# Performance work log

Measured on AMD Instinct MI355X. Metric: run time of the kernel, lower is better.

Reference implementation:

```python
import jax, jax.numpy as jnp
import numpy as np
from jax import lax

D_TEMPORAL, D_INNER, D_STATE, D_CONV, DT_RANK = 2, 4, 16, 4, 1
EPS = 1e-5


def setup_inputs() -> dict:
    key = jax.random.key(0)
    ks = jax.random.split(key, 14)
    B, L = 16, 32768
    f = lambda k, s, scale=1.0: jax.random.normal(k, s, jnp.float32) * scale
    dt_b = float(np.log(np.expm1(0.01)))  # softplus^-1(0.01), typical dt init
    A_log = jnp.log(jnp.tile(jnp.arange(1, D_STATE + 1, dtype=jnp.float32), (D_INNER, 1)))
    return {
        "hidden_states": f(ks[0], (B, D_TEMPORAL, L)),
        "norm_w": jnp.ones((D_TEMPORAL,), jnp.float32),
        "in_proj_w": f(ks[1], (2 * D_INNER, D_TEMPORAL), 0.5),
        "conv_w": f(ks[2], (D_INNER, D_CONV), 0.3),
        "conv_b": f(ks[3], (D_INNER,), 0.1),
        "x_proj_w": f(ks[4], (DT_RANK + 2 * D_STATE, D_INNER), 0.3),
        "dt_proj_w": f(ks[5], (D_INNER, DT_RANK), 1.0),
        "dt_proj_b": jnp.full((D_INNER,), dt_b, jnp.float32),
        "A_log": A_log,
        "D": jnp.ones((D_INNER,), jnp.float32),
        "conv_w_b": f(ks[6], (D_INNER, D_CONV), 0.3),
        "conv_b_b": f(ks[7], (D_INNER,), 0.1),
        "x_proj_w_b": f(ks[8], (DT_RANK + 2 * D_STATE, D_INNER), 0.3),
        "dt_proj_w_b": f(ks[9], (D_INNER, DT_RANK), 1.0),
        "dt_proj_b_b": jnp.full((D_INNER,), dt_b, jnp.float32),
        "A_b_log": A_log,
        "D_b": jnp.ones((D_INNER,), jnp.float32),
        "out_proj_w": f(ks[10], (D_TEMPORAL, D_INNER), 0.3),
        "norm_f_w": jnp.ones((D_TEMPORAL,), jnp.float32),
    }


def _silu(x):
    return x * jax.nn.sigmoid(x)


def _rmsnorm(x, w):
    return x * lax.rsqrt(jnp.mean(x * x, axis=-1, keepdims=True) + EPS) * w


def _branch(x, z, conv_w, conv_b, x_proj_w, dt_proj_w, dt_proj_b, A_log, D):
    # x, z: (B, d_inner, L). Causal depthwise conv + silu.
    Bb, d, L = x.shape
    xc = lax.conv_general_dilated(
        x, conv_w[:, None, :], (1,), [(D_CONV - 1, 0)],
        feature_group_count=d, dimension_numbers=("NCH", "OIH", "NCH"))
    u = _silu(xc + conv_b[None, :, None]).transpose(0, 2, 1)      # (B, L, d)
    x_dbl = u @ x_proj_w.T                                        # (B, L, rank+2n)
    dt, Bm, Cm = jnp.split(x_dbl, [DT_RANK, DT_RANK + D_STATE], axis=-1)
    dt = jax.nn.softplus(dt @ dt_proj_w.T + dt_proj_b)            # (B, L, d)
    A = -jnp.exp(A_log)                                           # (d, n)
    dA = jnp.exp(dt[..., None] * A)                               # (B, L, d, n)
    dBu = (dt * u)[..., None] * Bm[:, :, None, :]                 # (B, L, d, n)

    def step(h, inp):
        dA_t, dBu_t, C_t = inp
        h = dA_t * h + dBu_t                                      # (B, d, n)
        return h, jnp.einsum("bdn,bn->bd", h, C_t)

    h0 = jnp.zeros((Bb, d, D_STATE), dtype=u.dtype)
    _, ys = lax.scan(step, h0, (jnp.swapaxes(dA, 0, 1), jnp.swapaxes(dBu, 0, 1), jnp.swapaxes(Cm, 0, 1)))
    y = jnp.swapaxes(ys, 0, 1) + u * D                            # (B, L, d)
    return y * _silu(z.transpose(0, 2, 1))


def _forward(hidden_states, norm_w, in_proj_w, conv_w, conv_b, x_proj_w, dt_proj_w,
             dt_proj_b, A_log, D, conv_w_b, conv_b_b, x_proj_w_b, dt_proj_w_b,
             dt_proj_b_b, A_b_log, D_b, out_proj_w, norm_f_w):
    # hidden_states: (B, T=d_temporal, L); scan runs over L.
    hs = jnp.swapaxes(hidden_states, 1, 2)                        # (B, L, T)
    residual = hs.astype(jnp.float32)
    hs = _rmsnorm(residual, norm_w)
    xz = jnp.swapaxes(hs @ in_proj_w.T, 1, 2)                     # (B, 2*d_inner, L)
    x, z = jnp.split(xz, 2, axis=1)
    y_f = _branch(x, z, conv_w, conv_b, x_proj_w, dt_proj_w, dt_proj_b, A_log, D)
    y_b = _branch(x[..., ::-1], z[..., ::-1], conv_w_b, conv_b_b, x_proj_w_b,
                  dt_proj_w_b, dt_proj_b_b, A_b_log, D_b)
    y = y_f + y_b[:, ::-1, :]                                     # (B, L, d_inner)
    out = y @ out_proj_w.T                                        # (B, L, T)
    out = _rmsnorm(out + residual, norm_f_w)
    return jnp.swapaxes(out, 1, 2)                                # (B, T, L)


def reference(hidden_states, norm_w, in_proj_w, conv_w, conv_b, x_proj_w, dt_proj_w,
              dt_proj_b, A_log, D, conv_w_b, conv_b_b, x_proj_w_b, dt_proj_w_b,
              dt_proj_b_b, A_b_log, D_b, out_proj_w, norm_f_w):
    return _forward(hidden_states, norm_w, in_proj_w, conv_w, conv_b, x_proj_w,
                    dt_proj_w, dt_proj_b, A_log, D, conv_w_b, conv_b_b, x_proj_w_b,
                    dt_proj_w_b, dt_proj_b_b, A_b_log, D_b, out_proj_w, norm_f_w)
```

## Files before the change

kernel.cpp:

```cpp
#include <hip/hip_runtime.h>
#include <hip/hip_bf16.h>
#include <cstdint>

#define BB 16
#define LL 32768
#define NC 512

#define WD_SZ 256
#define XPW 0
#define CVW 132
#define CVB 148
#define DTW 152
#define DTB 156
#define AW  160
#define DW  224
#define G_INPROJ 512
#define G_NORMW 528
#define G_OUTP 530
#define G_NORMF 538
#define FLG 1000

#define PQ_OFF 4096
#define PQ_BYTES ((size_t)BB*2*NC*64*8)
#define HIN_OFF (PQ_OFF + PQ_BYTES)
#define HIN_BYTES ((size_t)BB*2*NC*64*4)
#define PLN_OFF (HIN_OFF + HIN_BYTES)
#define PLN_STRIDE 14336
#define PLN_BYTES ((size_t)BB*NC*PLN_STRIDE)

#define O_DTF 0
#define O_DTB 1088
#define O_DUF 2176
#define O_DUB 2752
#define O_BCF 3328
#define O_BCB 7680
#define O_ZS  12032
#define O_UD  13056

__device__ __forceinline__ float bf2f(unsigned short u){ return __uint_as_float(((unsigned int)u)<<16); }
__device__ __forceinline__ float blo(unsigned int u){ return __uint_as_float(u<<16); }
__device__ __forceinline__ float bhi(unsigned int u){ return __uint_as_float(u & 0xffff0000u); }
__device__ __forceinline__ unsigned short f2bf(float f){
  unsigned int x = __float_as_uint(f);
  x += 0x7fffu + ((x>>16)&1u);
  return (unsigned short)(x>>16);
}
__device__ __forceinline__ unsigned int pack2(float a, float b){
  __hip_bfloat162 h = __float22bfloat162_rn(make_float2(a,b));
  union { __hip_bfloat162 h2; unsigned int u; } cv; cv.h2 = h;
  return cv.u;
}
__device__ __forceinline__ float siluf(float x){
  return x * __builtin_amdgcn_rcpf(1.f + __expf(-x));
}
__device__ __forceinline__ float softplusf_(float x){
  return fmaxf(x,0.f) + 0.69314718056f*__log2f(1.f + __expf(-fabsf(x)));
}

__device__ __forceinline__ float rowsum16(float x){
  union { float f; int i; } a, t;
  a.f = x;
  t.i = __builtin_amdgcn_update_dpp(0, a.i, 0x121, 0xf, 0xf, true); a.f += t.f;
  t.i = __builtin_amdgcn_update_dpp(0, a.i, 0x122, 0xf, 0xf, true); a.f += t.f;
  t.i = __builtin_amdgcn_update_dpp(0, a.i, 0x124, 0xf, 0xf, true); a.f += t.f;
  t.i = __builtin_amdgcn_update_dpp(0, a.i, 0x128, 0xf, 0xf, true); a.f += t.f;
  return a.f;
}

__device__ __forceinline__ float ldw(const void* p, int i, int isf){
  return isf ? ((const float*)p)[i] : bf2f(((const unsigned short*)p)[i]);
}
__device__ __forceinline__ float2 hid2(const void* hid, int isf, int b, int t){
  if (isf){
    const float* p = (const float*)hid;
    return make_float2(p[(size_t)b*2*LL + t], p[(size_t)b*2*LL + LL + t]);
  }
  const unsigned short* p = (const unsigned short*)hid;
  return make_float2(bf2f(p[(size_t)b*2*LL + t]), bf2f(p[(size_t)b*2*LL + LL + t]));
}
__device__ __forceinline__ float4 xrow(const void* __restrict__ hid, int isf,
                                       const float* __restrict__ W, int b, int t){
  float2 h = hid2(hid, isf, b, t);
  float ms = rsqrtf(0.5f*(h.x*h.x + h.y*h.y) + 1e-5f);
  float v0 = h.x*ms*W[G_NORMW], v1 = h.y*ms*W[G_NORMW+1];
  float4 x;
  x.x = W[G_INPROJ+0]*v0 + W[G_INPROJ+1]*v1;
  x.y = W[G_INPROJ+2]*v0 + W[G_INPROJ+3]*v1;
  x.z = W[G_INPROJ+4]*v0 + W[G_INPROJ+5]*v1;
  x.w = W[G_INPROJ+6]*v0 + W[G_INPROJ+7]*v1;
  return x;
}

__device__ __forceinline__ void phaseA(const void* __restrict__ hid, int isf,
    const float* __restrict__ W, int b, int c, int lane,
    unsigned char* smem, float4* xb)
{
  float* dtF = (float*)(smem+O_DTF);
  float* dtB = (float*)(smem+O_DTB);
  unsigned short* duF = (unsigned short*)(smem+O_DUF);
  unsigned short* duB = (unsigned short*)(smem+O_DUB);
  unsigned int* BCF = (unsigned int*)(smem+O_BCF);
  unsigned int* BCB = (unsigned int*)(smem+O_BCB);
  float* zsP = (float*)(smem+O_ZS);
  float* uDP = (float*)(smem+O_UD);
  {
    int t = c*64 + lane;
    float2 h = hid2(hid, isf, b, t);
    float ms = rsqrtf(0.5f*(h.x*h.x + h.y*h.y) + 1e-5f);
    float v0 = h.x*ms*W[G_NORMW], v1 = h.y*ms*W[G_NORMW+1];
    float4 x;
    x.x = W[G_INPROJ+0]*v0 + W[G_INPROJ+1]*v1;
    x.y = W[G_INPROJ+2]*v0 + W[G_INPROJ+3]*v1;
    x.z = W[G_INPROJ+4]*v0 + W[G_INPROJ+5]*v1;
    x.w = W[G_INPROJ+6]*v0 + W[G_INPROJ+7]*v1;
    xb[lane+3] = x;
    float4 z4;
    z4.x = siluf(W[G_INPROJ+ 8]*v0 + W[G_INPROJ+ 9]*v1);
    z4.y = siluf(W[G_INPROJ+10]*v0 + W[G_INPROJ+11]*v1);
    z4.z = siluf(W[G_INPROJ+12]*v0 + W[G_INPROJ+13]*v1);
    z4.w = siluf(W[G_INPROJ+14]*v0 + W[G_INPROJ+15]*v1);
    *(float4*)&zsP[lane*4] = z4;
    if (lane < 3){
      int t2 = c*64 - 3 + lane;
      float4 v = make_float4(0.f,0.f,0.f,0.f);
      if (t2 >= 0) v = xrow(hid, isf, W, b, t2);
      xb[lane] = v;
    }
    if (lane >= 61){
      int t3 = c*64 + lane + 3;
      float4 v = make_float4(0.f,0.f,0.f,0.f);
      if (t3 < LL) v = xrow(hid, isf, W, b, t3);
      xb[lane+6] = v;
    }
  }
  __syncthreads();
  float4 xk0=xb[lane],xk1=xb[lane+1],xk2=xb[lane+2],xk3=xb[lane+3];
  float4 xk4=xb[lane+4],xk5=xb[lane+5],xk6=xb[lane+6];
  float uf[4], ub[4];
  uf[0] = siluf(W[CVB+0] + W[CVW+ 0]*xk0.x + W[CVW+ 1]*xk1.x + W[CVW+ 2]*xk2.x + W[CVW+ 3]*xk3.x);
  uf[1] = siluf(W[CVB+1] + W[CVW+ 4]*xk0.y + W[CVW+ 5]*xk1.y + W[CVW+ 6]*xk2.y + W[CVW+ 7]*xk3.y);
  uf[2] = siluf(W[CVB+2] + W[CVW+ 8]*xk0.z + W[CVW+ 9]*xk1.z + W[CVW+10]*xk2.z + W[CVW+11]*xk3.z);
  uf[3] = siluf(W[CVB+3] + W[CVW+12]*xk0.w + W[CVW+13]*xk1.w + W[CVW+14]*xk2.w + W[CVW+15]*xk3.w);
  const float* Wb = W + WD_SZ;
  ub[0] = siluf(Wb[CVB+0] + Wb[CVW+ 0]*xk6.x + Wb[CVW+ 1]*xk5.x + Wb[CVW+ 2]*xk4.x + Wb[CVW+ 3]*xk3.x);
  ub[1] = siluf(Wb[CVB+1] + Wb[CVW+ 4]*xk6.y + Wb[CVW+ 5]*xk5.y + Wb[CVW+ 6]*xk4.y + Wb[CVW+ 7]*xk3.y);
  ub[2] = siluf(Wb[CVB+2] + Wb[CVW+ 8]*xk6.z + Wb[CVW+ 9]*xk5.z + Wb[CVW+10]*xk4.z + Wb[CVW+11]*xk3.z);
  ub[3] = siluf(Wb[CVB+3] + Wb[CVW+12]*xk6.w + Wb[CVW+13]*xk5.w + Wb[CVW+14]*xk4.w + Wb[CVW+15]*xk3.w);
  *(float4*)&uDP[lane*4] = make_float4(
      uf[0]*W[DW+0]+ub[0]*Wb[DW+0], uf[1]*W[DW+1]+ub[1]*Wb[DW+1],
      uf[2]*W[DW+2]+ub[2]*Wb[DW+2], uf[3]*W[DW+3]+ub[3]*Wb[DW+3]);
  #pragma unroll
  for (int dr=0; dr<2; dr++){
    const float* Wd = W + dr*WD_SZ;
    const float* uu = dr ? ub : uf;
    float* dtp = dr ? dtB : dtF;
    unsigned short* dup = dr ? duB : duF;
    unsigned int* bcp = dr ? BCB : BCF;
    float dtr = Wd[XPW+0]*uu[0]+Wd[XPW+1]*uu[1]+Wd[XPW+2]*uu[2]+Wd[XPW+3]*uu[3];
    #pragma unroll
    for (int d2=0; d2<4; d2++){
      float dt = softplusf_(fmaf(Wd[DTW+d2], dtr, Wd[DTB+d2]));
      dtp[d2*68+lane] = dt;
      dup[d2*72+lane] = f2bf(dt*uu[d2]);
    }
    #pragma unroll
    for (int n=0;n<16;n++){
      float Bn = Wd[XPW+(1+n)*4+0]*uu[0]+Wd[XPW+(1+n)*4+1]*uu[1]
               + Wd[XPW+(1+n)*4+2]*uu[2]+Wd[XPW+(1+n)*4+3]*uu[3];
      float Cn = Wd[XPW+(17+n)*4+0]*uu[0]+Wd[XPW+(17+n)*4+1]*uu[1]
               + Wd[XPW+(17+n)*4+2]*uu[2]+Wd[XPW+(17+n)*4+3]*uu[3];
      bcp[n*68+lane] = pack2(Bn,Cn);
    }
  }
}

__global__ void k_prep(const void* __restrict__ normw, const void* __restrict__ inpj,
    const void* __restrict__ cwf, const void* __restrict__ cbf,
    const void* __restrict__ xpf, const void* __restrict__ dwf,
    const void* __restrict__ dbf, const void* __restrict__ alf,
    const void* __restrict__ ddf,
    const void* __restrict__ cwb, const void* __restrict__ cbb,
    const void* __restrict__ xpb, const void* __restrict__ dwb,
    const void* __restrict__ dbb, const void* __restrict__ alb,
    const void* __restrict__ ddb,
    const void* __restrict__ outp, const void* __restrict__ nfw,
    float* __restrict__ W)
{
  const int isf = (((const unsigned int*)ddf)[0] == 0x3F800000u) ? 1 : 0;
  int t = threadIdx.x;
  for (int i=t;i<132;i+=256){ W[XPW+i]=ldw(xpf,i,isf); W[WD_SZ+XPW+i]=ldw(xpb,i,isf); }
  for (int i=t;i<16;i+=256){ W[CVW+i]=ldw(cwf,i,isf); W[WD_SZ+CVW+i]=ldw(cwb,i,isf); W[G_INPROJ+i]=ldw(inpj,i,isf); }
  for (int i=t;i<4;i+=256){
    W[CVB+i]=ldw(cbf,i,isf); W[WD_SZ+CVB+i]=ldw(cbb,i,isf);
    W[DTW+i]=ldw(dwf,i,isf); W[WD_SZ+DTW+i]=ldw(dwb,i,isf);
    W[DTB+i]=ldw(dbf,i,isf); W[WD_SZ+DTB+i]=ldw(dbb,i,isf);
    W[DW+i] =ldw(ddf,i,isf); W[WD_SZ+DW+i] =ldw(ddb,i,isf);
  }
  for (int i=t;i<64;i+=256){
    W[AW+i]       = -__expf(ldw(alf,i,isf)) * 1.44269504089f;
    W[WD_SZ+AW+i] = -__expf(ldw(alb,i,isf)) * 1.44269504089f;
  }
  for (int i=t;i<8;i+=256) W[G_OUTP+i]=ldw(outp,i,isf);
  for (int i=t;i<2;i+=256){ W[G_NORMW+i]=ldw(normw,i,isf); W[G_NORMF+i]=ldw(nfw,i,isf); }
  if (t==0) W[FLG] = (float)isf;
}

template<bool SPL>
__global__ __launch_bounds__(64) void k_chunk(const void* __restrict__ hid,
    const float* __restrict__ W, float2* __restrict__ PQ,
    unsigned char* __restrict__ planes)
{
  __shared__ __align__(16) unsigned char smem[PLN_STRIDE];
  __shared__ __align__(16) float4 xb[70];
  const int lane = threadIdx.x;
  const int gid  = blockIdx.x;
  const int c    = gid & (NC-1);
  const int b    = gid >> 9;
  const int isf  = (int)W[FLG];

  phaseA(hid, isf, W, b, c, lane, smem, xb);
  __syncthreads();
  if (SPL){
    uint4* gp = (uint4*)(planes + (size_t)gid*PLN_STRIDE);
    const uint4* sp = (const uint4*)smem;
    #pragma unroll
    for (int i=0;i<14;i++) gp[i*64+lane] = sp[i*64+lane];
  }
  const float* dtF = (const float*)(smem+O_DTF);
  const float* dtB = (const float*)(smem+O_DTB);
  const unsigned short* duF = (const unsigned short*)(smem+O_DUF);
  const unsigned short* duB = (const unsigned short*)(smem+O_DUB);
  const unsigned int* BCF = (const unsigned int*)(smem+O_BCF);
  const unsigned int* BCB = (const unsigned int*)(smem+O_BCB);
  const int d = lane>>4, n = lane&15;
  const float Af = W[AW + d*16 + n];
  const float Ab = W[WD_SZ + AW + d*16 + n];
  float Pf=1.f, Qf=0.f, Pb=1.f, Qb=0.f;
  for (int j4=0; j4<16; j4++){
    const int t0f = j4*4, t0b = 60 - j4*4;
    float4 df4 = *(const float4*)&dtF[d*68+t0f];
    float4 db4 = *(const float4*)&dtB[d*68+t0b];
    uint2 uf2 = *(const uint2*)&duF[d*72+t0f];
    uint2 ub2 = *(const uint2*)&duB[d*72+t0b];
    uint4 cf4 = *(const uint4*)&BCF[n*68+t0f];
    uint4 cb4 = *(const uint4*)&BCB[n*68+t0b];
    float dfa[4]={df4.x,df4.y,df4.z,df4.w}, dba[4]={db4.x,db4.y,db4.z,db4.w};
    float duf[4]={blo(uf2.x),bhi(uf2.x),blo(uf2.y),bhi(uf2.y)};
    float dub[4]={blo(ub2.x),bhi(ub2.x),blo(ub2.y),bhi(ub2.y)};
    unsigned int cfa[4]={cf4.x,cf4.y,cf4.z,cf4.w}, cba[4]={cb4.x,cb4.y,cb4.z,cb4.w};
    #pragma unroll
    for (int jr=0; jr<4; jr++){
      float e = exp2f(Af*dfa[jr]);
      Pf *= e;
      Qf = fmaf(Qf, e, duf[jr]*blo(cfa[jr]));
      const int k = 3-jr;
      float eb = exp2f(Ab*dba[k]);
      Pb *= eb;
      Qb = fmaf(Qb, eb, dub[k]*blo(cba[k]));
    }
  }
  PQ[((size_t)(b*2+0)*NC + c)*64 + lane]        = make_float2(Pf,Qf);
  PQ[((size_t)(b*2+1)*NC + (NC-1-c))*64 + lane] = make_float2(Pb,Qb);
}

__global__ __launch_bounds__(256) void k_scan(const float2* __restrict__ PQ, float* __restrict__ hin)
{
  __shared__ float2 seg[4][64];
  const int bd = blockIdx.x;
  const int lane = threadIdx.x & 63;
  const int w = threadIdx.x >> 6;
  const size_t base = (size_t)bd*NC;
  const int c0 = w*128;
  float h = 0.f, R = 1.f;
  for (int cc=0; cc<128; cc+=16){
    float2 v[16];
    #pragma unroll
    for (int k=0;k<16;k++) v[k] = PQ[(base+c0+cc+k)*64+lane];
    #pragma unroll
    for (int k=0;k<16;k++){
      hin[(base+c0+cc+k)*64+lane] = h;
      h = fmaf(v[k].x, h, v[k].y);
      R *= v[k].x;
    }
  }
  seg[w][lane] = make_float2(R, h);
  __syncthreads();
  if (w > 0){
    float init = 0.f;
    #pragma unroll
    for (int s=0; s<3; s++){
      if (s < w){ float2 pq = seg[s][lane]; init = fmaf(pq.x, init, pq.y); }
    }
    float Rr = 1.f;
    for (int cc=0; cc<128; cc+=16){
      float pv[16], hv[16];
      #pragma unroll
      for (int k=0;k<16;k++) pv[k] = PQ[(base+c0+cc+k)*64+lane].x;
      #pragma unroll
      for (int k=0;k<16;k++) hv[k] = hin[(base+c0+cc+k)*64+lane];
      #pragma unroll
      for (int k=0;k<16;k++){
        hin[(base+c0+cc+k)*64+lane] = hv[k] + init*Rr;
        Rr *= pv[k];
      }
    }
  }
}

template<bool LPL>
__global__ __launch_bounds__(64) void k_fused(const void* __restrict__ hid,
    const float* __restrict__ W, const float* __restrict__ hin,
    const unsigned char* __restrict__ planes, void* __restrict__ out)
{
  __shared__ __align__(16) unsigned char smem[PLN_STRIDE];
  __shared__ __align__(16) float ySf[4][68];
  __shared__ __align__(16) float ySb[4][68];
  const int lane = threadIdx.x;
  const int gid  = blockIdx.x;
  const int c    = gid & (NC-1);
  const int b    = gid >> 9;
  const int isf  = (int)W[FLG];

  float hF = hin[((size_t)(b*2+0)*NC + c)*64 + lane];
  float hB = hin[((size_t)(b*2+1)*NC + (NC-1-c))*64 + lane];

  if constexpr (LPL){
    const uint4* gp = (const uint4*)(planes + (size_t)gid*PLN_STRIDE);
    uint4* sp = (uint4*)smem;
    #pragma unroll
    for (int i=0;i<14;i++) sp[i*64+lane] = gp[i*64+lane];
  } else {
    __shared__ __align__(16) float4 xb[70];
    phaseA(hid, isf, W, b, c, lane, smem, xb);
  }
  __syncthreads();

  const float* dtF = (const float*)(smem+O_DTF);
  const float* dtB = (const float*)(smem+O_DTB);
  const unsigned short* duF = (const unsigned short*)(smem+O_DUF);
  const unsigned short* duB = (const unsigned short*)(smem+O_DUB);
  const unsigned int* BCF = (const unsigned int*)(smem+O_BCF);
  const unsigned int* BCB = (const unsigned int*)(smem+O_BCB);
  const float* zsP = (const float*)(smem+O_ZS);
  const float* uDP = (const float*)(smem+O_UD);

  const int d = lane>>4, n = lane&15;
  const float Af = W[AW + d*16 + n];
  const float Ab = W[WD_SZ + AW + d*16 + n];
  for (int j4=0; j4<16; j4++){
    const int t0f = j4*4, t0b = 60 - j4*4;
    float4 df4 = *(const float4*)&dtF[d*68+t0f];
    float4 db4 = *(const float4*)&dtB[d*68+t0b];
    uint2 uf2 = *(const uint2*)&duF[d*72+t0f];
    uint2 ub2 = *(const uint2*)&duB[d*72+t0b];
    uint4 cf4 = *(const uint4*)&BCF[n*68+t0f];
    uint4 cb4 = *(const uint4*)&BCB[n*68+t0b];
    float dfa[4]={df4.x,df4.y,df4.z,df4.w}, dba[4]={db4.x,db4.y,db4.z,db4.w};
    float duf[4]={blo(uf2.x),bhi(uf2.x),blo(uf2.y),bhi(uf2.y)};
    float dub[4]={blo(ub2.x),bhi(ub2.x),blo(ub2.y),bhi(ub2.y)};
    unsigned int cfa[4]={cf4.x,cf4.y,cf4.z,cf4.w}, cba[4]={cb4.x,cb4.y,cb4.z,cb4.w};
    float sF[4], sB[4];
    #pragma unroll
    for (int jr=0; jr<4; jr++){
      float e = exp2f(Af*dfa[jr]);
      hF = fmaf(e, hF, duf[jr]*blo(cfa[jr]));
      sF[jr] = rowsum16(hF*bhi(cfa[jr]));
      const int k = 3-jr;
      float eb = exp2f(Ab*dba[k]);
      hB = fmaf(eb, hB, dub[k]*blo(cba[k]));
      sB[k] = rowsum16(hB*bhi(cba[k]));
    }
    if (n == 0){
      *(float4*)&ySf[d][t0f] = make_float4(sF[0],sF[1],sF[2],sF[3]);
      *(float4*)&ySb[d][t0b] = make_float4(sB[0],sB[1],sB[2],sB[3]);
    }
  }
  __syncthreads();
  {
    int t = c*64 + lane;
    float4 zz = *(const float4*)&zsP[lane*4];
    float4 ud = *(const float4*)&uDP[lane*4];
    float y0 = (ySf[0][lane] + ySb[0][lane] + ud.x) * zz.x;
    float y1 = (ySf[1][lane] + ySb[1][lane] + ud.y) * zz.y;
    float y2 = (ySf[2][lane] + ySb[2][lane] + ud.z) * zz.z;
    float y3 = (ySf[3][lane] + ySb[3][lane] + ud.w) * zz.w;
    float o0 = W[G_OUTP+0]*y0 + W[G_OUTP+1]*y1 + W[G_OUTP+2]*y2 + W[G_OUTP+3]*y3;
    float o1 = W[G_OUTP+4]*y0 + W[G_OUTP+5]*y1 + W[G_OUTP+6]*y2 + W[G_OUTP+7]*y3;
    float2 r = hid2(hid, isf, b, t);
    o0 += r.x;
    o1 += r.y;
    float ms = rsqrtf(0.5f*(o0*o0 + o1*o1) + 1e-5f);
    float e0 = o0*ms*W[G_NORMF], e1 = o1*ms*W[G_NORMF+1];
    size_t i0 = (size_t)b*2*LL + t, i1 = i0 + LL;
    if (isf){
      ((float*)out)[i0] = e0;
      ((float*)out)[i1] = e1;
    } else {
      ((unsigned short*)out)[i0] = f2bf(e0);
      ((unsigned short*)out)[i1] = f2bf(e1);
    }
  }
}

extern "C" void kernel_launch(void* const* d_in, const int* in_sizes, int n_in,
                              void* d_out, int out_size, void* d_ws, size_t ws_size,
                              hipStream_t stream)
{
  (void)in_sizes; (void)n_in; (void)out_size;
  const void* hid   = d_in[0];
  float* W   = (float*)d_ws;
  float2* PQ = (float2*)((char*)d_ws + PQ_OFF);
  float* hin = (float*)((char*)d_ws + HIN_OFF);
  unsigned char* planes = (unsigned char*)d_ws + PLN_OFF;

  k_prep<<<1,256,0,stream>>>(d_in[1], d_in[2], d_in[3], d_in[4], d_in[5], d_in[6],
                             d_in[7], d_in[8], d_in[9], d_in[10], d_in[11], d_in[12],
                             d_in[13], d_in[14], d_in[15], d_in[16], d_in[17], d_in[18], W);
  const bool useP = ws_size >= (size_t)(PLN_OFF + PLN_BYTES);
  if (useP){
    k_chunk<true><<<BB*NC, 64, 0, stream>>>(hid, W, PQ, planes);
    k_scan<<<BB*2, 256, 0, stream>>>(PQ, hin);
    k_fused<true><<<BB*NC, 64, 0, stream>>>(hid, W, hin, planes, d_out);
  } else {
    k_chunk<false><<<BB*NC, 64, 0, stream>>>(hid, W, PQ, planes);
    k_scan<<<BB*2, 256, 0, stream>>>(PQ, hin);
    k_fused<false><<<BB*NC, 64, 0, stream>>>(hid, W, hin, planes, d_out);
  }
}
```

Measured before the change: 207.4 us.

## Pack dt and dt*u as bf16 pairs and read planes directly from global

Stores dt and dt*u together as a packed bf16 pair, dropping the separate fp32 dt array. This shrinks the per-chunk plane written to and read from workspace, and the scan loops now unpack both values from one word. The plane-reading fused kernel no longer copies the plane into shared memory; it reads dt/u and B/C straight from global memory inside the scan loop. Rounding dt to bf16 adds precision loss in the exponent argument, and uncoalesced per-lane global reads (rows indexed by n) may cost more than the removed LDS staging.

```diff
diff --git a/kernel.cpp b/kernel.cpp
--- a/kernel.cpp
+++ b/kernel.cpp
@@ -25,17 +25,15 @@
 #define HIN_OFF (PQ_OFF + PQ_BYTES)
 #define HIN_BYTES ((size_t)BB*2*NC*64*4)
 #define PLN_OFF (HIN_OFF + HIN_BYTES)
-#define PLN_STRIDE 14336
+#define PLN_STRIDE 13312
 #define PLN_BYTES ((size_t)BB*NC*PLN_STRIDE)
 
-#define O_DTF 0
-#define O_DTB 1088
-#define O_DUF 2176
-#define O_DUB 2752
-#define O_BCF 3328
-#define O_BCB 7680
-#define O_ZS  12032
-#define O_UD  13056
+#define O_DUF 0
+#define O_DUB 1088
+#define O_BCF 2176
+#define O_BCB 6528
+#define O_ZS  10880
+#define O_UD  11904
 
 __device__ __forceinline__ float bf2f(unsigned short u){ return __uint_as_float(((unsigned int)u)<<16); }
 __device__ __forceinline__ float blo(unsigned int u){ return __uint_as_float(u<<16); }
@@ -95,10 +93,8 @@
     const float* __restrict__ W, int b, int c, int lane,
     unsigned char* smem, float4* xb)
 {
-  float* dtF = (float*)(smem+O_DTF);
-  float* dtB = (float*)(smem+O_DTB);
-  unsigned short* duF = (unsigned short*)(smem+O_DUF);
-  unsigned short* duB = (unsigned short*)(smem+O_DUB);
+  unsigned int* DUF = (unsigned int*)(smem+O_DUF);
+  unsigned int* DUB = (unsigned int*)(smem+O_DUB);
   unsigned int* BCF = (unsigned int*)(smem+O_BCF);
   unsigned int* BCB = (unsigned int*)(smem+O_BCB);
   float* zsP = (float*)(smem+O_ZS);
@@ -153,15 +149,13 @@
   for (int dr=0; dr<2; dr++){
     const float* Wd = W + dr*WD_SZ;
     const float* uu = dr ? ub : uf;
-    float* dtp = dr ? dtB : dtF;
-    unsigned short* dup = dr ? duB : duF;
+    unsigned int* dup = dr ? DUB : DUF;
     unsigned int* bcp = dr ? BCB : BCF;
     float dtr = Wd[XPW+0]*uu[0]+Wd[XPW+1]*uu[1]+Wd[XPW+2]*uu[2]+Wd[XPW+3]*uu[3];
     #pragma unroll
     for (int d2=0; d2<4; d2++){
       float dt = softplusf_(fmaf(Wd[DTW+d2], dtr, Wd[DTB+d2]));
-      dtp[d2*68+lane] = dt;
-      dup[d2*72+lane] = f2bf(dt*uu[d2]);
+      dup[d2*68+lane] = pack2(dt, dt*uu[d2]);
     }
     #pragma unroll
     for (int n=0;n<16;n++){
@@ -224,12 +218,10 @@
     uint4* gp = (uint4*)(planes + (size_t)gid*PLN_STRIDE);
     const uint4* sp = (const uint4*)smem;
     #pragma unroll
-    for (int i=0;i<14;i++) gp[i*64+lane] = sp[i*64+lane];
-  }
-  const float* dtF = (const float*)(smem+O_DTF);
-  const float* dtB = (const float*)(smem+O_DTB);
-  const unsigned short* duF = (const unsigned short*)(smem+O_DUF);
-  const unsigned short* duB = (const unsigned short*)(smem+O_DUB);
+    for (int i=0;i<13;i++) gp[i*64+lane] = sp[i*64+lane];
+  }
+  const unsigned int* DUF = (const unsigned int*)(smem+O_DUF);
+  const unsigned int* DUB = (const unsigned int*)(smem+O_DUB);
   const unsigned int* BCF = (const unsigned int*)(smem+O_BCF);
   const unsigned int* BCB = (const unsigned int*)(smem+O_BCB);
   const int d = lane>>4, n = lane&15;
@@ -238,25 +230,21 @@
   float Pf=1.f, Qf=0.f, Pb=1.f, Qb=0.f;
   for (int j4=0; j4<16; j4++){
     const int t0f = j4*4, t0b = 60 - j4*4;
-    float4 df4 = *(const float4*)&dtF[d*68+t0f];
-    float4 db4 = *(const float4*)&dtB[d*68+t0b];
-    uint2 uf2 = *(const uint2*)&duF[d*72+t0f];
-    uint2 ub2 = *(const uint2*)&duB[d*72+t0b];
+    uint4 uf4 = *(const uint4*)&DUF[d*68+t0f];
+    uint4 ub4 = *(const uint4*)&DUB[d*68+t0b];
     uint4 cf4 = *(const uint4*)&BCF[n*68+t0f];
     uint4 cb4 = *(const uint4*)&BCB[n*68+t0b];
-    float dfa[4]={df4.x,df4.y,df4.z,df4.w}, dba[4]={db4.x,db4.y,db4.z,db4.w};
-    float duf[4]={blo(uf2.x),bhi(uf2.x),blo(uf2.y),bhi(uf2.y)};
-    float dub[4]={blo(ub2.x),bhi(ub2.x),blo(ub2.y),bhi(ub2.y)};
+    unsigned int ufa[4]={uf4.x,uf4.y,uf4.z,uf4.w}, uba[4]={ub4.x,ub4.y,ub4.z,ub4.w};
     unsigned int cfa[4]={cf4.x,cf4.y,cf4.z,cf4.w}, cba[4]={cb4.x,cb4.y,cb4.z,cb4.w};
     #pragma unroll
     for (int jr=0; jr<4; jr++){
-      float e = exp2f(Af*dfa[jr]);
+      float e = exp2f(Af*blo(ufa[jr]));
       Pf *= e;
-      Qf = fmaf(Qf, e, duf[jr]*blo(cfa[jr]));
+      Qf = fmaf(Qf, e, bhi(ufa[jr])*blo(cfa[jr]));
       const int k = 3-jr;
-      float eb = exp2f(Ab*dba[k]);
+      float eb = exp2f(Ab*blo(uba[k]));
       Pb *= eb;
-      Qb = fmaf(Qb, eb, dub[k]*blo(cba[k]));
+      Qb = fmaf(Qb, eb, bhi(uba[k])*blo(cba[k]));
     }
   }
   PQ[((size_t)(b*2+0)*NC + c)*64 + lane]        = make_float2(Pf,Qf);
@@ -307,12 +295,10 @@
   }
 }
 
-template<bool LPL>
-__global__ __launch_bounds__(64) void k_fused(const void* __restrict__ hid,
+__global__ __launch_bounds__(64) void k_fusedP(const void* __restrict__ hid,
     const float* __restrict__ W, const float* __restrict__ hin,
     const unsigned char* __restrict__ planes, void* __restrict__ out)
 {
-  __shared__ __align__(16) unsigned char smem[PLN_STRIDE];
   __shared__ __align__(16) float ySf[4][68];
   __shared__ __align__(16) float ySb[4][68];
   const int lane = threadIdx.x;
@@ -324,50 +310,113 @@
   float hF = hin[((size_t)(b*2+0)*NC + c)*64 + lane];
   float hB = hin[((size_t)(b*2+1)*NC + (NC-1-c))*64 + lane];
 
-  if constexpr (LPL){
-    const uint4* gp = (const uint4*)(planes + (size_t)gid*PLN_STRIDE);
-    uint4* sp = (uint4*)smem;
-    #pragma unroll
-    for (int i=0;i<14;i++) sp[i*64+lane] = gp[i*64+lane];
-  } else {
-    __shared__ __align__(16) float4 xb[70];
-    phaseA(hid, isf, W, b, c, lane, smem, xb);
-  }
-  __syncthreads();
-
-  const float* dtF = (const float*)(smem+O_DTF);
-  const float* dtB = (const float*)(smem+O_DTB);
-  const unsigned short* duF = (const unsigned short*)(smem+O_DUF);
-  const unsigned short* duB = (const unsigned short*)(smem+O_DUB);
-  const unsigned int* BCF = (const unsigned int*)(smem+O_BCF);
-  const unsigned int* BCB = (const unsigned int*)(smem+O_BCB);
-  const float* zsP = (const float*)(smem+O_ZS);
-  const float* uDP = (const float*)(smem+O_UD);
+  const unsigned char* pg = planes + (size_t)gid*PLN_STRIDE;
+  const unsigned int* DUF = (const unsigned int*)(pg+O_DUF);
+  const unsigned int* DUB = (const unsigned int*)(pg+O_DUB);
+  const unsigned int* BCF = (const unsigned int*)(pg+O_BCF);
+  const unsigned int* BCB = (const unsigned int*)(pg+O_BCB);
 
   const int d = lane>>4, n = lane&15;
   const float Af = W[AW + d*16 + n];
   const float Ab = W[WD_SZ + AW + d*16 + n];
   for (int j4=0; j4<16; j4++){
     const int t0f = j4*4, t0b = 60 - j4*4;
-    float4 df4 = *(const float4*)&dtF[d*68+t0f];
-    float4 db4 = *(const float4*)&dtB[d*68+t0b];
-    uint2 uf2 = *(const uint2*)&duF[d*72+t0f];
-    uint2 ub2 = *(const uint2*)&duB[d*72+t0b];
+    uint4 uf4 = *(const uint4*)&DUF[d*68+t0f];
+    uint4 ub4 = *(const uint4*)&DUB[d*68+t0b];
     uint4 cf4 = *(const uint4*)&BCF[n*68+t0f];
     uint4 cb4 = *(const uint4*)&BCB[n*68+t0b];
-    float dfa[4]={df4.x,df4.y,df4.z,df4.w}, dba[4]={db4.x,db4.y,db4.z,db4.w};
-    float duf[4]={blo(uf2.x),bhi(uf2.x),blo(uf2.y),bhi(uf2.y)};
-    float dub[4]={blo(ub2.x),bhi(ub2.x),blo(ub2.y),bhi(ub2.y)};
+    unsigned int ufa[4]={uf4.x,uf4.y,uf4.z,uf4.w}, uba[4]={ub4.x,ub4.y,ub4.z,ub4.w};
     unsigned int cfa[4]={cf4.x,cf4.y,cf4.z,cf4.w}, cba[4]={cb4.x,cb4.y,cb4.z,cb4.w};
     float sF[4], sB[4];
     #pragma unroll
     for (int jr=0; jr<4; jr++){
-      float e = exp2f(Af*dfa[jr]);
-      hF = fmaf(e, hF, duf[jr]*blo(cfa[jr]));
+      float e = exp2f(Af*blo(ufa[jr]));
+      hF = fmaf(e, hF, bhi(ufa[jr])*blo(cfa[jr]));
       sF[jr] = rowsum16(hF*bhi(cfa[jr]));
       const int k = 3-jr;
-      float eb = exp2f(Ab*dba[k]);
-      hB = fmaf(eb, hB, dub[k]*blo(cba[k]));
+      float eb = exp2f(Ab*blo(uba[k]));
+      hB = fmaf(eb, hB, bhi(uba[k])*blo(cba[k]));
+      sB[k] = rowsum16(hB*bhi(cba[k]));
+    }
+    if (n == 0){
+      *(float4*)&ySf[d][t0f] = make_float4(sF[0],sF[1],sF[2],sF[3]);
+      *(float4*)&ySb[d][t0b] = make_float4(sB[0],sB[1],sB[2],sB[3]);
+    }
+  }
+  __syncthreads();
+  {
+    int t = c*64 + lane;
+    float4 zz = *(const float4*)(pg + O_ZS + lane*16);
+    float4 ud = *(const float4*)(pg + O_UD + lane*16);
+    float y0 = (ySf[0][lane] + ySb[0][lane] + ud.x) * zz.x;
+    float y1 = (ySf[1][lane] + ySb[1][lane] + ud.y) * zz.y;
+    float y2 = (ySf[2][lane] + ySb[2][lane] + ud.z) * zz.z;
+    float y3 = (ySf[3][lane] + ySb[3][lane] + ud.w) * zz.w;
+    float o0 = W[G_OUTP+0]*y0 + W[G_OUTP+1]*y1 + W[G_OUTP+2]*y2 + W[G_OUTP+3]*y3;
+    float o1 = W[G_OUTP+4]*y0 + W[G_OUTP+5]*y1 + W[G_OUTP+6]*y2 + W[G_OUTP+7]*y3;
+    float2 r = hid2(hid, isf, b, t);
+    o0 += r.x;
+    o1 += r.y;
+    float ms = rsqrtf(0.5f*(o0*o0 + o1*o1) + 1e-5f);
+    float e0 = o0*ms*W[G_NORMF], e1 = o1*ms*W[G_NORMF+1];
+    size_t i0 = (size_t)b*2*LL + t, i1 = i0 + LL;
+    if (isf){
+      ((float*)out)[i0] = e0;
+      ((float*)out)[i1] = e1;
+    } else {
+      ((unsigned short*)out)[i0] = f2bf(e0);
+      ((unsigned short*)out)[i1] = f2bf(e1);
+    }
+  }
+}
+
+__global__ __launch_bounds__(64) void k_fusedF(const void* __restrict__ hid,
+    const float* __restrict__ W, const float* __restrict__ hin,
+    void* __restrict__ out)
+{
+  __shared__ __align__(16) unsigned char smem[PLN_STRIDE];
+  __shared__ __align__(16) float4 xb[70];
+  __shared__ __align__(16) float ySf[4][68];
+  __shared__ __align__(16) float ySb[4][68];
+  const int lane = threadIdx.x;
+  const int gid  = blockIdx.x;
+  const int c    = gid & (NC-1);
+  const int b    = gid >> 9;
+  const int isf  = (int)W[FLG];
+
+  float hF = hin[((size_t)(b*2+0)*NC + c)*64 + lane];
+  float hB = hin[((size_t)(b*2+1)*NC + (NC-1-c))*64 + lane];
+
+  phaseA(hid, isf, W, b, c, lane, smem, xb);
+  __syncthreads();
+
+  const unsigned int* DUF = (const unsigned int*)(smem+O_DUF);
+  const unsigned int* DUB = (const unsigned int*)(smem+O_DUB);
+  const unsigned int* BCF = (const unsigned int*)(smem+O_BCF);
+  const unsigned int* BCB = (const unsigned int*)(smem+O_BCB);
+  const float* zsP = (const float*)(smem+O_ZS);
+  const float* uDP = (const float*)(smem+O_UD);
+
+  const int d = lane>>4, n = lane&15;
+  const float Af = W[AW + d*16 + n];
+  const float Ab = W[WD_SZ + AW + d*16 + n];
+  for (int j4=0; j4<16; j4++){
+    const int t0f = j4*4, t0b = 60 - j4*4;
+    uint4 uf4 = *(const uint4*)&DUF[d*68+t0f];
+    uint4 ub4 = *(const uint4*)&DUB[d*68+t0b];
+    uint4 cf4 = *(const uint4*)&BCF[n*68+t0f];
+    uint4 cb4 = *(const uint4*)&BCB[n*68+t0b];
+    unsigned int ufa[4]={uf4.x,uf4.y,uf4.z,uf4.w}, uba[4]={ub4.x,ub4.y,ub4.z,ub4.w};
+    unsigned int cfa[4]={cf4.x,cf4.y,cf4.z,cf4.w}, cba[4]={cb4.x,cb4.y,cb4.z,cb4.w};
+    float sF[4], sB[4];
+    #pragma unroll
+    for (int jr=0; jr<4; jr++){
+      float e = exp2f(Af*blo(ufa[jr]));
+      hF = fmaf(e, hF, bhi(ufa[jr])*blo(cfa[jr]));
+      sF[jr] = rowsum16(hF*bhi(cfa[jr]));
+      const int k = 3-jr;
+      float eb = exp2f(Ab*blo(uba[k]));
+      hB = fmaf(eb, hB, bhi(uba[k])*blo(cba[k]));
       sB[k] = rowsum16(hB*bhi(cba[k]));
     }
     if (n == 0){
@@ -420,10 +469,10 @@
   if (useP){
     k_chunk<true><<<BB*NC, 64, 0, stream>>>(hid, W, PQ, planes);
     k_scan<<<BB*2, 256, 0, stream>>>(PQ, hin);
-    k_fused<true><<<BB*NC, 64, 0, stream>>>(hid, W, hin, planes, d_out);
+    k_fusedP<<<BB*NC, 64, 0, stream>>>(hid, W, hin, planes, d_out);
   } else {
     k_chunk<false><<<BB*NC, 64, 0, stream>>>(hid, W, PQ, planes);
     k_scan<<<BB*2, 256, 0, stream>>>(PQ, hin);
-    k_fused<false><<<BB*NC, 64, 0, stream>>>(hid, W, hin, planes, d_out);
-  }
-}
+    k_fusedF<<<BB*NC, 64, 0, stream>>>(hid, W, hin, d_out);
+  }
+}
```

After: 222.8 us. +7.4%, slower.
